# Performance work log

Hardware: AMD Instinct MI355X
Metric: run time of the kernel (lower is better)

Reference implementation:

```python
import jax, jax.numpy as jnp
import numpy as np

BATCH, IN_F, OUT_F = 65536, 1024, 256


def setup_inputs() -> dict:
    key = jax.random.key(0)
    kx, kw, kb, ks = jax.random.split(key, 4)
    x = jax.random.normal(kx, (BATCH, IN_F), dtype=jnp.float32)
    # ternary weight in {-1, 0, 1}, shape [out, in] as in F.linear
    weight = jax.random.randint(kw, (OUT_F, IN_F), -1, 2).astype(jnp.float32)
    # bias is integer-valued (floor'd in get_sign_bias_from_bn)
    bias = jax.random.randint(kb, (OUT_F,), -64, 64).astype(jnp.float32)
    # sign in {-1, +1}, broadcast shape [1, out]
    sign = (jax.random.randint(ks, (1, OUT_F), 0, 2).astype(jnp.float32) * 2.0 - 1.0)
    return {"x": x, "weight": weight, "bias": bias, "sign": sign}


def reference(x, weight, bias, sign):
    # y = F.linear(x, W, b); rounding=True -> round; then threshold by sign
    y = jnp.round(jnp.dot(x, weight.T) + bias)  # [B, out]
    return jnp.where(y * sign >= 0, jnp.float32(1.0), jnp.float32(0.0)).astype(x.dtype)
```

## Files before the change

### kernel.cpp

```cpp
#include <hip/hip_runtime.h>
#include <hip/hip_bf16.h>

#define M_BATCH 65536
#define K_IN    1024
#define N_OUT   256
#define TAU     0.015f

#define CNT_BOFF 524288ULL
#define WL_BOFF  524544ULL
#define WL_CAP   1048576ULL
#define WS_NEED  (WL_BOFF + WL_CAP * 4ULL)

typedef __attribute__((ext_vector_type(8))) short short8;
typedef __attribute__((ext_vector_type(4))) short short4v;
typedef __attribute__((ext_vector_type(4))) float f32x4;

__device__ inline short f2bf(float f) {
    __hip_bfloat16 h = __float2bfloat16(f);
    return __builtin_bit_cast(short, h);
}
__device__ inline float bf2f(short s) {
    unsigned u = ((unsigned)(unsigned short)s) << 16;
    return __builtin_bit_cast(float, u);
}

__device__ inline float c3_score(const float* __restrict__ xr_,
                                 const float* __restrict__ wr_) {
    float a0 = 0.f, a1 = 0.f;
    float4 xc0 = *(const float4*)(xr_);
    float4 wc0 = *(const float4*)(wr_);
    float4 xc1 = *(const float4*)(xr_ + 512);
    float4 wc1 = *(const float4*)(wr_ + 512);
    for (int k4 = 0; k4 < 128; ++k4) {
        const int kn = (k4 + 1) & 127;
        const float4 nx0 = *(const float4*)(xr_ + kn * 4);
        const float4 nw0 = *(const float4*)(wr_ + kn * 4);
        const float4 nx1 = *(const float4*)(xr_ + 512 + kn * 4);
        const float4 nw1 = *(const float4*)(wr_ + 512 + kn * 4);
        a0 = fmaf(xc0.x, wc0.x, a0); a1 = fmaf(xc1.x, wc1.x, a1);
        a0 = fmaf(xc0.y, wc0.y, a0); a1 = fmaf(xc1.y, wc1.y, a1);
        a0 = fmaf(xc0.z, wc0.z, a0); a1 = fmaf(xc1.z, wc1.z, a1);
        a0 = fmaf(xc0.w, wc0.w, a0); a1 = fmaf(xc1.w, wc1.w, a1);
        xc0 = nx0; wc0 = nw0; xc1 = nx1; wc1 = nw1;
    }
    return a0 + a1;
}

__global__ __launch_bounds__(512) void wconv21(const float* __restrict__ w,
                                               short* __restrict__ wt,
                                               unsigned* __restrict__ counter) {
    if (blockIdx.x == 0 && threadIdx.x == 0) *counter = 0u;
    const int idx = blockIdx.x * 512 + threadIdx.x;
    const float4 v = ((const float4*)w)[idx];
    short4v h;
    h.x = f2bf(v.x); h.y = f2bf(v.y); h.z = f2bf(v.z); h.w = f2bf(v.w);
    ((short4v*)wt)[idx] = h;
}

__global__ __launch_bounds__(256) void binlin_f21(const float* __restrict__ x,
                                                  const float* __restrict__ wf,
                                                  const short* __restrict__ wt,
                                                  const float* __restrict__ bias,
                                                  const float* __restrict__ sign,
                                                  float* __restrict__ out,
                                                  unsigned* __restrict__ counter,
                                                  unsigned* __restrict__ wl) {
    __shared__ __align__(16) unsigned char dec[16384];

    const int bid     = blockIdx.x;
    const int logical = (bid & 7) * 128 + (bid >> 3);
    const int m0 = (logical >> 1) * 128;
    const int n0 = (logical & 1) * 128;

    const int tid  = threadIdx.x;
    const int lane = tid & 63;
    const int wid  = tid >> 6;
    const int wm   = wid >> 1;
    const int wn   = wid & 1;
    const int l15  = lane & 15;
    const int l4   = lane >> 4;

    const float* abase = x  + (size_t)(m0 + wm * 64 + l15) * K_IN + l4 * 8;
    const short* bbase = wt + (size_t)(n0 + wn * 64 + l15) * K_IN + l4 * 8;

    f32x4 acc[4][4];
#pragma unroll
    for (int i = 0; i < 4; ++i)
#pragma unroll
        for (int j = 0; j < 4; ++j) acc[i][j] = (f32x4){0.f, 0.f, 0.f, 0.f};

    for (int kt = 0; kt < 16; ++kt) {
#pragma unroll
        for (int kk = 0; kk < 2; ++kk) {
            const int ko = kt * 64 + kk * 32;
            short8 bfr[4];
#pragma unroll
            for (int ni = 0; ni < 4; ++ni)
                bfr[ni] = *(const short8*)(bbase + (size_t)ni * 16 * K_IN + ko);
#pragma unroll
            for (int mi = 0; mi < 4; ++mi) {
                const float4 f0 = *(const float4*)(abase + (size_t)mi * 16 * K_IN + ko);
                const float4 f1 = *(const float4*)(abase + (size_t)mi * 16 * K_IN + ko + 4);
                const float fv[8] = {f0.x, f0.y, f0.z, f0.w, f1.x, f1.y, f1.z, f1.w};
                short8 ahi, alo;
#pragma unroll
                for (int e = 0; e < 8; ++e) {
                    const short h = f2bf(fv[e]);
                    ahi[e] = h;
                    alo[e] = f2bf(fv[e] - bf2f(h));
                }
#pragma unroll
                for (int ni = 0; ni < 4; ++ni) {
                    acc[mi][ni] = __builtin_amdgcn_mfma_f32_16x16x32_bf16(
                        ahi, bfr[ni], acc[mi][ni], 0, 0, 0);
                    acc[mi][ni] = __builtin_amdgcn_mfma_f32_16x16x32_bf16(
                        alo, bfr[ni], acc[mi][ni], 0, 0, 0);
                }
            }
        }
    }

#pragma unroll
    for (int ni = 0; ni < 4; ++ni) {
        const int nl = wn * 64 + ni * 16 + l15;
        const int n  = n0 + nl;
        const float b = bias[n];
        const float s = sign[n];
#pragma unroll
        for (int mi = 0; mi < 4; ++mi) {
            const int ml = wm * 64 + mi * 16 + l4 * 4;
#pragma unroll
            for (int j = 0; j < 4; ++j) {
                const float t = (acc[mi][ni][j] + b) * s;
                unsigned char d = (t >= -0.5f) ? 1 : 0;
                if (fabsf(t + 0.5f) < TAU) {
                    const int m = m0 + ml + j;
                    const unsigned idx = atomicAdd(counter, 1u);
                    if (idx < WL_CAP) {
                        wl[idx] = ((unsigned)m << 8) | (unsigned)n;
                    } else {
                        const float cs = c3_score(x + (size_t)m * K_IN,
                                                  wf + (size_t)n * K_IN);
                        d = (((cs + b) * s) >= -0.5f) ? 1 : 0;
                    }
                }
                dec[(ml + j) * 128 + nl] = d;
            }
        }
    }
    __syncthreads();

#pragma unroll
    for (int it = 0; it < 16; ++it) {
        const int f   = it * 256 + tid;
        const int row = f >> 5;
        const int c4  = f & 31;
        const uchar4 dv = *(const uchar4*)&dec[row * 128 + c4 * 4];
        *(float4*)(out + (size_t)(m0 + row) * N_OUT + n0 + c4 * 4) =
            make_float4((float)dv.x, (float)dv.y, (float)dv.z, (float)dv.w);
    }
}

__global__ __launch_bounds__(256) void fixwl21(const float* __restrict__ x,
                                               const float* __restrict__ wf,
                                               const float* __restrict__ bias,
                                               const float* __restrict__ sign,
                                               const unsigned* __restrict__ counter,
                                               const unsigned* __restrict__ wl,
                                               float* __restrict__ out) {
    const unsigned count = min(*counter, (unsigned)WL_CAP);
    const unsigned stride = gridDim.x * 256;
    for (unsigned i = blockIdx.x * 256 + threadIdx.x; i < count; i += stride) {
        const unsigned code = wl[i];
        const int m = (int)(code >> 8);
        const int n = (int)(code & 255u);
        const float cs = c3_score(x + (size_t)m * K_IN, wf + (size_t)n * K_IN);
        const float tt = (cs + bias[n]) * sign[n];
        out[(size_t)m * N_OUT + n] = (tt >= -0.5f) ? 1.0f : 0.0f;
    }
}

__global__ __launch_bounds__(256) void binlin_fast(const float* __restrict__ x,
                                                   const float* __restrict__ w,
                                                   const float* __restrict__ bias,
                                                   const float* __restrict__ sign,
                                                   float* __restrict__ out) {
    __shared__ float As[32][132];
    __shared__ float Bs2[32][132];
    const int tid = threadIdx.x;
    const int tx  = tid & 15;
    const int ty  = tid >> 4;
    const int n0  = blockIdx.x * 128;
    const int m0  = blockIdx.y * 128;
    const int sr  = tid >> 3;
    const int sc  = (tid & 7) * 4;
    float acc[8][8];
#pragma unroll
    for (int i = 0; i < 8; ++i)
#pragma unroll
        for (int j = 0; j < 8; ++j) acc[i][j] = 0.f;
    for (int kt = 0; kt < K_IN; kt += 32) {
        __syncthreads();
#pragma unroll
        for (int q = 0; q < 4; ++q) {
            const int row = sr + q * 32;
            const float4 va = *(const float4*)(x + (size_t)(m0 + row) * K_IN + kt + sc);
            As[sc + 0][row] = va.x; As[sc + 1][row] = va.y;
            As[sc + 2][row] = va.z; As[sc + 3][row] = va.w;
            const float4 vb = *(const float4*)(w + (size_t)(n0 + row) * K_IN + kt + sc);
            Bs2[sc + 0][row] = vb.x; Bs2[sc + 1][row] = vb.y;
            Bs2[sc + 2][row] = vb.z; Bs2[sc + 3][row] = vb.w;
        }
        __syncthreads();
#pragma unroll
        for (int kk = 0; kk < 32; ++kk) {
            const float4 a0 = *(const float4*)&As[kk][ty * 8];
            const float4 a1 = *(const float4*)&As[kk][ty * 8 + 4];
            const float4 b0 = *(const float4*)&Bs2[kk][tx * 8];
            const float4 b1 = *(const float4*)&Bs2[kk][tx * 8 + 4];
            const float a[8] = {a0.x, a0.y, a0.z, a0.w, a1.x, a1.y, a1.z, a1.w};
            const float b[8] = {b0.x, b0.y, b0.z, b0.w, b1.x, b1.y, b1.z, b1.w};
#pragma unroll
            for (int i = 0; i < 8; ++i)
#pragma unroll
                for (int j = 0; j < 8; ++j)
                    acc[i][j] = fmaf(a[i], b[j], acc[i][j]);
        }
    }
    const int nb = n0 + tx * 8;
    float bv[8], sv[8];
#pragma unroll
    for (int j = 0; j < 8; ++j) { bv[j] = bias[nb + j]; sv[j] = sign[nb + j]; }
#pragma unroll
    for (int i = 0; i < 8; ++i) {
        const int m = m0 + ty * 8 + i;
        float o[8];
#pragma unroll
        for (int j = 0; j < 8; ++j) {
            const float t = (acc[i][j] + bv[j]) * sv[j];
            if (fabsf(t + 0.5f) < TAU) {
                const float cs = c3_score(x + (size_t)m * K_IN,
                                          w + (size_t)(nb + j) * K_IN);
                o[j] = (((cs + bv[j]) * sv[j]) >= -0.5f) ? 1.0f : 0.0f;
            } else {
                o[j] = (t >= -0.5f) ? 1.0f : 0.0f;
            }
        }
        float4* op = (float4*)(out + (size_t)m * N_OUT + nb);
        op[0] = make_float4(o[0], o[1], o[2], o[3]);
        op[1] = make_float4(o[4], o[5], o[6], o[7]);
    }
}

extern "C" void kernel_launch(void* const* d_in, const int* in_sizes, int n_in,
                              void* d_out, int out_size, void* d_ws, size_t ws_size,
                              hipStream_t stream) {
    const float* x    = (const float*)d_in[0];
    const float* w    = (const float*)d_in[1];
    const float* bias = (const float*)d_in[2];
    const float* sign = (const float*)d_in[3];

    if (n_in >= 4 && in_sizes[0] != M_BATCH * K_IN) {
        const float* small[2] = {nullptr, nullptr};
        int nsmall = 0;
        for (int i = 0; i < 4; ++i) {
            if (in_sizes[i] == M_BATCH * K_IN)      x = (const float*)d_in[i];
            else if (in_sizes[i] == N_OUT * K_IN)   w = (const float*)d_in[i];
            else if (nsmall < 2) small[nsmall++] = (const float*)d_in[i];
        }
        if (nsmall == 2) { bias = small[0]; sign = small[1]; }
    }

    float* out = (float*)d_out;

    if (ws_size >= WS_NEED) {
        short*    wtp = (short*)d_ws;
        unsigned* cnt = (unsigned*)((char*)d_ws + CNT_BOFF);
        unsigned* wl  = (unsigned*)((char*)d_ws + WL_BOFF);

        wconv21<<<128, 512, 0, stream>>>(w, wtp, cnt);
        binlin_f21<<<1024, 256, 0, stream>>>(x, w, wtp, bias, sign, out, cnt, wl);
        fixwl21<<<256, 256, 0, stream>>>(x, w, bias, sign, cnt, wl, out);
    } else {
        dim3 grid(N_OUT / 128, M_BATCH / 128);
        binlin_fast<<<grid, 256, 0, stream>>>(x, w, bias, sign, out);
    }
}
```

Measured before the change: 311.2 us.

## Double-buffer GEMM operand tiles in LDS via direct global-to-LDS loads

Replaces per-thread direct global loads of x and bf16 weight fragments with cooperative global_load_lds staging into two LDS buffers, using an XOR swizzle to avoid bank conflicts. The next k-slice is loaded while the current slice is computed, and operands are shared across waves instead of each wave fetching from global/L2. This adds 48KB of LDS per block, which may reduce occupancy, plus barriers per k-step. There is also a question of whether global_load_lds completion is properly waited on before the barrier.

```diff
diff --git a/kernel.cpp b/kernel.cpp
--- a/kernel.cpp
+++ b/kernel.cpp
@@ -11,6 +11,11 @@
 #define WL_CAP   1048576ULL
 #define WS_NEED  (WL_BOFF + WL_CAP * 4ULL)
 
+#define A0_OFF 0
+#define A1_OFF 16384
+#define B0_OFF 32768
+#define B1_OFF 40960
+
 typedef __attribute__((ext_vector_type(8))) short short8;
 typedef __attribute__((ext_vector_type(4))) short short4v;
 typedef __attribute__((ext_vector_type(4))) float f32x4;
@@ -22,6 +27,11 @@
 __device__ inline float bf2f(short s) {
     unsigned u = ((unsigned)(unsigned short)s) << 16;
     return __builtin_bit_cast(float, u);
+}
+__device__ inline void gload16(const void* g, void* lds) {
+    __builtin_amdgcn_global_load_lds(
+        (const __attribute__((address_space(1))) unsigned int*)g,
+        (__attribute__((address_space(3))) unsigned int*)lds, 16, 0, 0);
 }
 
 __device__ inline float c3_score(const float* __restrict__ xr_,
@@ -46,7 +56,7 @@
     return a0 + a1;
 }
 
-__global__ __launch_bounds__(512) void wconv21(const float* __restrict__ w,
+__global__ __launch_bounds__(512) void wconv22(const float* __restrict__ w,
                                                short* __restrict__ wt,
                                                unsigned* __restrict__ counter) {
     if (blockIdx.x == 0 && threadIdx.x == 0) *counter = 0u;
@@ -57,15 +67,15 @@
     ((short4v*)wt)[idx] = h;
 }
 
-__global__ __launch_bounds__(256) void binlin_f21(const float* __restrict__ x,
-                                                  const float* __restrict__ wf,
-                                                  const short* __restrict__ wt,
-                                                  const float* __restrict__ bias,
-                                                  const float* __restrict__ sign,
-                                                  float* __restrict__ out,
-                                                  unsigned* __restrict__ counter,
-                                                  unsigned* __restrict__ wl) {
-    __shared__ __align__(16) unsigned char dec[16384];
+__global__ __launch_bounds__(256) void binlin_db22(const float* __restrict__ x,
+                                                   const float* __restrict__ wf,
+                                                   const short* __restrict__ wt,
+                                                   const float* __restrict__ bias,
+                                                   const float* __restrict__ sign,
+                                                   float* __restrict__ out,
+                                                   unsigned* __restrict__ counter,
+                                                   unsigned* __restrict__ wl) {
+    __shared__ __align__(16) unsigned char smem[49152];
 
     const int bid     = blockIdx.x;
     const int logical = (bid & 7) * 128 + (bid >> 3);
@@ -80,8 +90,32 @@
     const int l15  = lane & 15;
     const int l4   = lane >> 4;
 
-    const float* abase = x  + (size_t)(m0 + wm * 64 + l15) * K_IN + l4 * 8;
-    const short* bbase = wt + (size_t)(n0 + wn * 64 + l15) * K_IN + l4 * 8;
+    size_t xs0, xs1, xs2, xs3;
+    {
+        const int r  = lane >> 3;
+        const int cp = (lane & 7) ^ ((r & 3) << 1);
+#define XSRC(q) ((size_t)(m0 + wid * 32 + (q) * 8 + r) * K_IN + cp * 4)
+        xs0 = XSRC(0); xs1 = XSRC(1); xs2 = XSRC(2); xs3 = XSRC(3);
+#undef XSRC
+    }
+    size_t bs0, bs1;
+    {
+        const int r  = lane >> 2;
+        const int cp = (lane & 3) ^ (r & 3);
+        bs0 = (size_t)(n0 + wid * 32 + 0 * 16 + r) * K_IN + cp * 8;
+        bs1 = (size_t)(n0 + wid * 32 + 1 * 16 + r) * K_IN + cp * 8;
+    }
+    const int xd0 = (wid * 32 + 0) * 128, xd1 = (wid * 32 + 8) * 128;
+    const int xd2 = (wid * 32 + 16) * 128, xd3 = (wid * 32 + 24) * 128;
+    const int bd0 = (wid * 32 + 0) * 64,  bd1 = (wid * 32 + 16) * 64;
+
+#define STAGE(AOFF, BOFF, KT) {                                         \
+        gload16(x + xs0 + (KT) * 32, smem + (AOFF) + xd0);              \
+        gload16(x + xs1 + (KT) * 32, smem + (AOFF) + xd1);              \
+        gload16(x + xs2 + (KT) * 32, smem + (AOFF) + xd2);              \
+        gload16(x + xs3 + (KT) * 32, smem + (AOFF) + xd3);              \
+        gload16(wt + bs0 + (KT) * 32, smem + (BOFF) + bd0);             \
+        gload16(wt + bs1 + (KT) * 32, smem + (BOFF) + bd1);             }
 
     f32x4 acc[4][4];
 #pragma unroll
@@ -89,37 +123,51 @@
 #pragma unroll
         for (int j = 0; j < 4; ++j) acc[i][j] = (f32x4){0.f, 0.f, 0.f, 0.f};
 
-    for (int kt = 0; kt < 16; ++kt) {
-#pragma unroll
-        for (int kk = 0; kk < 2; ++kk) {
-            const int ko = kt * 64 + kk * 32;
-            short8 bfr[4];
-#pragma unroll
-            for (int ni = 0; ni < 4; ++ni)
-                bfr[ni] = *(const short8*)(bbase + (size_t)ni * 16 * K_IN + ko);
-#pragma unroll
-            for (int mi = 0; mi < 4; ++mi) {
-                const float4 f0 = *(const float4*)(abase + (size_t)mi * 16 * K_IN + ko);
-                const float4 f1 = *(const float4*)(abase + (size_t)mi * 16 * K_IN + ko + 4);
-                const float fv[8] = {f0.x, f0.y, f0.z, f0.w, f1.x, f1.y, f1.z, f1.w};
-                short8 ahi, alo;
-#pragma unroll
-                for (int e = 0; e < 8; ++e) {
-                    const short h = f2bf(fv[e]);
-                    ahi[e] = h;
-                    alo[e] = f2bf(fv[e] - bf2f(h));
-                }
-#pragma unroll
-                for (int ni = 0; ni < 4; ++ni) {
-                    acc[mi][ni] = __builtin_amdgcn_mfma_f32_16x16x32_bf16(
-                        ahi, bfr[ni], acc[mi][ni], 0, 0, 0);
-                    acc[mi][ni] = __builtin_amdgcn_mfma_f32_16x16x32_bf16(
-                        alo, bfr[ni], acc[mi][ni], 0, 0, 0);
-                }
-            }
-        }
-    }
-
+#define COMPUTE(AOFF, BOFF) {                                           \
+        short8 bfr[4];                                                  \
+        _Pragma("unroll")                                               \
+        for (int ni = 0; ni < 4; ++ni) {                                \
+            const int Rn = wn * 64 + ni * 16 + l15;                     \
+            bfr[ni] = *(const short8*)(smem + (BOFF) + Rn * 64 +        \
+                                       ((l4 ^ (Rn & 3)) << 4));         \
+        }                                                               \
+        _Pragma("unroll")                                               \
+        for (int mi = 0; mi < 4; ++mi) {                                \
+            const int Rm  = wm * 64 + mi * 16 + l15;                    \
+            const int cp0 = (l4 * 2) ^ ((Rm & 3) << 1);                 \
+            const float4 f0 = *(const float4*)(smem + (AOFF) + Rm * 128 + cp0 * 16); \
+            const float4 f1 = *(const float4*)(smem + (AOFF) + Rm * 128 + cp0 * 16 + 16); \
+            const float fv[8] = {f0.x, f0.y, f0.z, f0.w, f1.x, f1.y, f1.z, f1.w}; \
+            short8 ahi, alo;                                            \
+            _Pragma("unroll")                                           \
+            for (int e = 0; e < 8; ++e) {                               \
+                const short h = f2bf(fv[e]);                            \
+                ahi[e] = h;                                             \
+                alo[e] = f2bf(fv[e] - bf2f(h));                         \
+            }                                                           \
+            _Pragma("unroll")                                           \
+            for (int ni = 0; ni < 4; ++ni) {                            \
+                acc[mi][ni] = __builtin_amdgcn_mfma_f32_16x16x32_bf16(  \
+                    ahi, bfr[ni], acc[mi][ni], 0, 0, 0);                \
+                acc[mi][ni] = __builtin_amdgcn_mfma_f32_16x16x32_bf16(  \
+                    alo, bfr[ni], acc[mi][ni], 0, 0, 0);                \
+            }                                                           \
+        }                                                               }
+
+    STAGE(A0_OFF, B0_OFF, 0)
+    __syncthreads();
+
+    for (int it = 0; it < 16; ++it) {
+        const int kt = it * 2;
+        if (kt + 1 < 32) STAGE(A1_OFF, B1_OFF, kt + 1)
+        COMPUTE(A0_OFF, B0_OFF)
+        __syncthreads();
+        if (kt + 2 < 32) STAGE(A0_OFF, B0_OFF, kt + 2)
+        COMPUTE(A1_OFF, B1_OFF)
+        __syncthreads();
+    }
+
+    unsigned char* dec = smem;
 #pragma unroll
     for (int ni = 0; ni < 4; ++ni) {
         const int nl = wn * 64 + ni * 16 + l15;
@@ -161,7 +209,7 @@
     }
 }
 
-__global__ __launch_bounds__(256) void fixwl21(const float* __restrict__ x,
+__global__ __launch_bounds__(256) void fixwl22(const float* __restrict__ x,
                                                const float* __restrict__ wf,
                                                const float* __restrict__ bias,
                                                const float* __restrict__ sign,
@@ -278,9 +326,9 @@
         unsigned* cnt = (unsigned*)((char*)d_ws + CNT_BOFF);
         unsigned* wl  = (unsigned*)((char*)d_ws + WL_BOFF);
 
-        wconv21<<<128, 512, 0, stream>>>(w, wtp, cnt);
-        binlin_f21<<<1024, 256, 0, stream>>>(x, w, wtp, bias, sign, out, cnt, wl);
-        fixwl21<<<256, 256, 0, stream>>>(x, w, bias, sign, cnt, wl, out);
+        wconv22<<<128, 512, 0, stream>>>(w, wtp, cnt);
+        binlin_db22<<<1024, 256, 0, stream>>>(x, w, wtp, bias, sign, out, cnt, wl);
+        fixwl22<<<256, 256, 0, stream>>>(x, w, bias, sign, cnt, wl, out);
     } else {
         dim3 grid(N_OUT / 128, M_BATCH / 128);
         binlin_fast<<<grid, 256, 0, stream>>>(x, w, bias, sign, out);
```

Measured after the change: 307.3 us. Within noise of the previous version (-1.2%).
